# Optimization experiments

Measured on AMD Instinct MI355X. Metric: run time of the kernel, lower is better.

Reference implementation:

```python
import jax, jax.numpy as jnp
import numpy as np

BATCH, N_NEURONS = 4096, 4096
FEAT = 512
MAP_H, MAP_W = 256, 256
M = MAP_H * MAP_W
TAU_MEM = 20.0
THRESHOLD = 1.0
LR = 0.005          # stdp_params['learning_rate']
SIGMA = 2.0         # SOM neighborhood radius (grid units)
N_UPDATES = 3       # perceive() runs the SOM forward+update loop 3 times


def setup_inputs() -> dict:
    key = jax.random.key(0)
    k = jax.random.split(key, 6)
    return {
        "sensory_input": jax.random.uniform(k[0], (BATCH, N_NEURONS), dtype=jnp.float32),
        "W_in":  jax.random.normal(k[1], (N_NEURONS, FEAT), dtype=jnp.float32) * 0.02,
        "W_out": jax.random.normal(k[2], (FEAT, FEAT), dtype=jnp.float32) * 0.05,
        "proj_W": jax.random.normal(k[3], (FEAT, FEAT), dtype=jnp.float32) * 0.05,
        "proj_b": jax.random.normal(k[4], (FEAT,), dtype=jnp.float32) * 0.05,
        "som_w": jax.random.uniform(k[5], (M, FEAT), dtype=jnp.float32),
    }


def _grid_coords():
    yy, xx = jnp.meshgrid(jnp.arange(MAP_H, dtype=jnp.float32),
                          jnp.arange(MAP_W, dtype=jnp.float32), indexing="ij")
    return jnp.stack([yy.ravel(), xx.ravel()], axis=-1)  # [M, 2]


def reference(sensory_input, W_in, W_out, proj_W, proj_b, som_w):
    # --- CorticalColumn (single LIF step, prev state None -> v0 = 0) ---
    x = sensory_input.mean(axis=0)                  # [N] batch mean per perceive()
    current = x @ W_in                              # [FEAT] feedforward current
    v = current                                     # v = 0*decay + current
    spikes = (v >= THRESHOLD).astype(v.dtype)       # LIF threshold, hard reset
    v_after = jnp.where(spikes > 0, 0.0, v)
    out_ff = spikes @ W_out                         # column feedforward output [FEAT]

    # --- input projection + ReLU ---
    feat = jax.nn.relu(out_ff @ proj_W.T + proj_b)  # [FEAT]

    coords = _grid_coords()                         # [M, 2]

    def som_act(w):
        d2 = jnp.sum((w - feat) ** 2, axis=-1)      # [M] distance sweep (memory-bound)
        return jnp.exp(-d2 / (2.0 * FEAT))          # rate-coded activation

    def step(w, _):
        act = som_act(w)
        bmu = jnp.argmax(act)                       # best matching unit
        g2 = jnp.sum((coords - coords[bmu]) ** 2, axis=-1)
        nb = jnp.exp(-g2 / (2.0 * SIGMA ** 2))      # Gaussian neighborhood
        w = w + LR * nb[:, None] * (feat - w)       # STDP-style pull toward input
        return w, None

    som_w, _ = jax.lax.scan(step, som_w, None, length=N_UPDATES)

    final = som_act(som_w).reshape(MAP_H, MAP_W)    # final SOM activation map
    return final
```

## Files before the change

kernel.cpp:

```cpp
#include <hip/hip_runtime.h>

#define NN        4096
#define FEATN     512
#define LRC       0.005f


__global__ void k_colsum_part(const float* __restrict__ A, float* __restrict__ partial, int rpb) {
    int col = blockIdx.x * 1024 + threadIdx.x * 4;
    const float* p = A + (size_t)blockIdx.y * rpb * NN + col;
    float4 acc = make_float4(0.f, 0.f, 0.f, 0.f);
    for (int r = 0; r < rpb; r += 8) {
        #pragma unroll
        for (int u = 0; u < 8; ++u) {
            float4 v = *reinterpret_cast<const float4*>(p + (size_t)(r + u) * NN);
            acc.x += v.x; acc.y += v.y; acc.z += v.z; acc.w += v.w;
        }
    }
    *reinterpret_cast<float4*>(partial + (size_t)blockIdx.y * NN + col) = acc;
}

__global__ void k_colsum_fin(const float* __restrict__ partial, float* __restrict__ sumx,
                             float* __restrict__ current, float* __restrict__ outff,
                             unsigned long long* __restrict__ bmuKey, int chunks) {
    int col = blockIdx.x * 256 + threadIdx.x;
    float acc = 0.f;
    #pragma unroll 8
    for (int p = 0; p < chunks; ++p)
        acc += partial[(size_t)p * NN + col];
    sumx[col] = acc * (1.0f / 4096.0f);
    if (blockIdx.x == 0) { current[threadIdx.x] = 0.f; current[threadIdx.x + 256] = 0.f; }
    if (blockIdx.x == 1) { outff[threadIdx.x]   = 0.f; outff[threadIdx.x + 256]   = 0.f; }
    if (blockIdx.x == 2 && threadIdx.x == 0) *bmuKey = ~0ull;
}

__global__ void k_current(const float* __restrict__ Win, const float* __restrict__ sumx,
                          float* __restrict__ current) {
    int t  = blockIdx.y * 256 + threadIdx.x;
    int i0 = blockIdx.x * 64;
    float acc = 0.f;
    #pragma unroll 8
    for (int i = 0; i < 64; ++i)
        acc += sumx[i0 + i] * Win[(size_t)(i0 + i) * FEATN + t];
    atomicAdd(&current[t], acc);
}

__global__ void k_outff(const float* __restrict__ Wout, const float* __restrict__ current,
                        float* __restrict__ outff) {
    int t  = blockIdx.y * 256 + threadIdx.x;
    int k0 = blockIdx.x * 32;
    float acc = 0.f;
    for (int k = 0; k < 32; ++k) {
        if (current[k0 + k] >= 1.0f)
            acc += Wout[(size_t)(k0 + k) * FEATN + t];
    }
    atomicAdd(&outff[t], acc);
}

__global__ void k_feat(const float* __restrict__ projW, const float* __restrict__ projb,
                       const float* __restrict__ outff, float* __restrict__ feat) {
    int lane = threadIdx.x & 63;
    int j    = blockIdx.x * 4 + (threadIdx.x >> 6);
    const float4* row = reinterpret_cast<const float4*>(projW + (size_t)j * FEATN);
    const float4* v   = reinterpret_cast<const float4*>(outff);
    float4 a0 = row[lane],      b0 = v[lane];
    float4 a1 = row[lane + 64], b1 = v[lane + 64];
    float s = a0.x * b0.x + a0.y * b0.y + a0.z * b0.z + a0.w * b0.w
            + a1.x * b1.x + a1.y * b1.y + a1.z * b1.z + a1.w * b1.w;
    #pragma unroll
    for (int k = 32; k >= 1; k >>= 1) s += __shfl_xor(s, k, 64);
    if (lane == 0) {
        float f = s + projb[j];
        feat[j] = f > 0.f ? f : 0.f;
    }
}

__global__ void k_d2(const float* __restrict__ somw, const float* __restrict__ feat,
                     float* __restrict__ d2out, unsigned long long* __restrict__ bmuKey) {
    __shared__ float sf[FEATN];
    __shared__ unsigned long long smin[4];
    int tid = threadIdx.x;
    sf[tid]       = feat[tid];
    sf[tid + 256] = feat[tid + 256];
    __syncthreads();

    int wave = tid >> 6, lane = tid & 63;
    int base = blockIdx.x * 32 + wave * 8;
    const float4* fv = reinterpret_cast<const float4*>(sf);
    float4 f0 = fv[lane], f1 = fv[lane + 64];

    float4 va[8], vb[8];
    #pragma unroll
    for (int r = 0; r < 8; ++r) {
        const float4* row = reinterpret_cast<const float4*>(somw + (size_t)(base + r) * FEATN);
        va[r] = row[lane];
        vb[r] = row[lane + 64];
    }

    float s[8];
    #pragma unroll
    for (int r = 0; r < 8; ++r) {
        float d, acc = 0.f;
        d = va[r].x - f0.x; acc += d * d;
        d = va[r].y - f0.y; acc += d * d;
        d = va[r].z - f0.z; acc += d * d;
        d = va[r].w - f0.w; acc += d * d;
        d = vb[r].x - f1.x; acc += d * d;
        d = vb[r].y - f1.y; acc += d * d;
        d = vb[r].z - f1.z; acc += d * d;
        d = vb[r].w - f1.w; acc += d * d;
        s[r] = acc;
    }
    #pragma unroll
    for (int r = 0; r < 8; ++r) {
        #pragma unroll
        for (int k = 32; k >= 1; k >>= 1) s[r] += __shfl_xor(s[r], k, 64);
    }

    if (lane == 0) {
        float4 o0 = make_float4(s[0], s[1], s[2], s[3]);
        float4 o1 = make_float4(s[4], s[5], s[6], s[7]);
        *reinterpret_cast<float4*>(d2out + base)     = o0;
        *reinterpret_cast<float4*>(d2out + base + 4) = o1;
        unsigned long long kmin = ~0ull;
        #pragma unroll
        for (int r = 0; r < 8; ++r) {
            unsigned long long key =
                ((unsigned long long)__float_as_uint(s[r]) << 32) | (unsigned)(base + r);
            if (key < kmin) kmin = key;
        }
        smin[wave] = kmin;
    }
    __syncthreads();
    if (tid == 0) {
        unsigned long long k0 = smin[0];
        if (smin[1] < k0) k0 = smin[1];
        if (smin[2] < k0) k0 = smin[2];
        if (smin[3] < k0) k0 = smin[3];
        if (k0 < *(volatile unsigned long long*)bmuKey)
            atomicMin(bmuKey, k0);
    }
}

__global__ void k_final(float* __restrict__ out, const unsigned long long* __restrict__ bmuKey) {
    int m = blockIdx.x * 256 + threadIdx.x;
    unsigned long long key = *bmuKey;
    int bmu = (int)(key & 0xFFFFFFFFull);
    float dy = (float)(m >> 8)  - (float)(bmu >> 8);
    float dx = (float)(m & 255) - (float)(bmu & 255);
    float g2 = dy * dy + dx * dx;
    float nb = expf(-g2 * 0.125f);
    float fac = 1.0f - LRC * nb;
    float f2 = fac * fac;
    float f6 = f2 * f2 * f2;
    float d2 = out[m];
    out[m] = expf(-(d2 * f6) * (1.0f / 1024.0f));
}

extern "C" void kernel_launch(void* const* d_in, const int* in_sizes, int n_in,
                              void* d_out, int out_size, void* d_ws, size_t ws_size,
                              hipStream_t stream) {
    const float* sensory = (const float*)d_in[0];
    const float* Win     = (const float*)d_in[1];
    const float* Wout    = (const float*)d_in[2];
    const float* projW   = (const float*)d_in[3];
    const float* projb   = (const float*)d_in[4];
    const float* somw    = (const float*)d_in[5];
    float* out = (float*)d_out;

    char* ws = (char*)d_ws;
    float* sumx    = (float*)(ws);
    float* current = (float*)(ws + 16384);
    float* outff   = (float*)(ws + 18432);
    float* feat    = (float*)(ws + 20480);
    unsigned long long* bmuKey = (unsigned long long*)(ws + 22528);
    float* partial = (float*)(ws + 24576);

    int chunks = 128;
    while (chunks > 16 && ws_size < (size_t)24576 + (size_t)chunks * NN * 4) chunks >>= 1;
    int rpb = NN / chunks;

    hipLaunchKernelGGL(k_colsum_part, dim3(4, chunks), dim3(256), 0, stream, sensory, partial, rpb);
    hipLaunchKernelGGL(k_colsum_fin,  dim3(16),        dim3(256), 0, stream, partial, sumx, current, outff, bmuKey, chunks);
    hipLaunchKernelGGL(k_current,     dim3(64, 2),     dim3(256), 0, stream, Win, sumx, current);
    hipLaunchKernelGGL(k_outff,       dim3(16, 2),     dim3(256), 0, stream, Wout, current, outff);
    hipLaunchKernelGGL(k_feat,        dim3(128),       dim3(256), 0, stream, projW, projb, outff, feat);
    hipLaunchKernelGGL(k_d2,          dim3(2048),      dim3(256), 0, stream, somw, feat, out, bmuKey);
    hipLaunchKernelGGL(k_final,       dim3(256),       dim3(256), 0, stream, out, bmuKey);
}
```

Baseline: 277.3 us.

## Fuse front-end column kernels into one persistent kernel with grid barriers

Replaces the five front-end launches (column sum partials, final reduction, W_in matvec, W_out spike matvec, projection) with a single 256-block kernel that separates the phases with software grid barriers built on atomic counters and flags. The goal is to remove per-launch overhead and the inter-kernel gaps in the serial chain of small matvecs. Barrier counters are cleared each call with a memset. The partial-sum layout is fixed at 64 chunks, and the barriers only work if all 256 blocks are resident at once, which would deadlock otherwise.

```diff
diff --git a/kernel.cpp b/kernel.cpp
--- a/kernel.cpp
+++ b/kernel.cpp
@@ -1,76 +1,109 @@
 #include <hip/hip_runtime.h>
 
-#define NN        4096
-#define FEATN     512
-#define LRC       0.005f
-
-
-__global__ void k_colsum_part(const float* __restrict__ A, float* __restrict__ partial, int rpb) {
-    int col = blockIdx.x * 1024 + threadIdx.x * 4;
-    const float* p = A + (size_t)blockIdx.y * rpb * NN + col;
-    float4 acc = make_float4(0.f, 0.f, 0.f, 0.f);
-    for (int r = 0; r < rpb; r += 8) {
-        #pragma unroll
-        for (int u = 0; u < 8; ++u) {
-            float4 v = *reinterpret_cast<const float4*>(p + (size_t)(r + u) * NN);
-            acc.x += v.x; acc.y += v.y; acc.z += v.z; acc.w += v.w;
-        }
-    }
-    *reinterpret_cast<float4*>(partial + (size_t)blockIdx.y * NN + col) = acc;
-}
-
-__global__ void k_colsum_fin(const float* __restrict__ partial, float* __restrict__ sumx,
-                             float* __restrict__ current, float* __restrict__ outff,
-                             unsigned long long* __restrict__ bmuKey, int chunks) {
-    int col = blockIdx.x * 256 + threadIdx.x;
-    float acc = 0.f;
-    #pragma unroll 8
-    for (int p = 0; p < chunks; ++p)
-        acc += partial[(size_t)p * NN + col];
-    sumx[col] = acc * (1.0f / 4096.0f);
-    if (blockIdx.x == 0) { current[threadIdx.x] = 0.f; current[threadIdx.x + 256] = 0.f; }
-    if (blockIdx.x == 1) { outff[threadIdx.x]   = 0.f; outff[threadIdx.x + 256]   = 0.f; }
-    if (blockIdx.x == 2 && threadIdx.x == 0) *bmuKey = ~0ull;
-}
-
-__global__ void k_current(const float* __restrict__ Win, const float* __restrict__ sumx,
-                          float* __restrict__ current) {
-    int t  = blockIdx.y * 256 + threadIdx.x;
-    int i0 = blockIdx.x * 64;
-    float acc = 0.f;
-    #pragma unroll 8
-    for (int i = 0; i < 64; ++i)
-        acc += sumx[i0 + i] * Win[(size_t)(i0 + i) * FEATN + t];
-    atomicAdd(&current[t], acc);
-}
-
-__global__ void k_outff(const float* __restrict__ Wout, const float* __restrict__ current,
-                        float* __restrict__ outff) {
-    int t  = blockIdx.y * 256 + threadIdx.x;
-    int k0 = blockIdx.x * 32;
-    float acc = 0.f;
-    for (int k = 0; k < 32; ++k) {
-        if (current[k0 + k] >= 1.0f)
-            acc += Wout[(size_t)(k0 + k) * FEATN + t];
-    }
-    atomicAdd(&outff[t], acc);
-}
-
-__global__ void k_feat(const float* __restrict__ projW, const float* __restrict__ projb,
-                       const float* __restrict__ outff, float* __restrict__ feat) {
-    int lane = threadIdx.x & 63;
-    int j    = blockIdx.x * 4 + (threadIdx.x >> 6);
-    const float4* row = reinterpret_cast<const float4*>(projW + (size_t)j * FEATN);
-    const float4* v   = reinterpret_cast<const float4*>(outff);
-    float4 a0 = row[lane],      b0 = v[lane];
-    float4 a1 = row[lane + 64], b1 = v[lane + 64];
-    float s = a0.x * b0.x + a0.y * b0.y + a0.z * b0.z + a0.w * b0.w
-            + a1.x * b1.x + a1.y * b1.y + a1.z * b1.z + a1.w * b1.w;
-    #pragma unroll
-    for (int k = 32; k >= 1; k >>= 1) s += __shfl_xor(s, k, 64);
-    if (lane == 0) {
-        float f = s + projb[j];
-        feat[j] = f > 0.f ? f : 0.f;
+#define NNEUR 4096
+#define FEATN 512
+#define LRC   0.005f
+#define NBLK  256
+
+
+__device__ __forceinline__ void gbar(unsigned* bar, int k) {
+    __syncthreads();
+    if (threadIdx.x == 0) {
+        __threadfence();
+        unsigned prev = atomicAdd(&bar[k], 1u);
+        if (prev == NBLK - 1u) {
+            __hip_atomic_store(&bar[4 + k], 1u, __ATOMIC_RELEASE, __HIP_MEMORY_SCOPE_AGENT);
+        } else {
+            while (__hip_atomic_load(&bar[4 + k], __ATOMIC_ACQUIRE, __HIP_MEMORY_SCOPE_AGENT) == 0u)
+                __builtin_amdgcn_s_sleep(2);
+        }
+        __threadfence();
+    }
+    __syncthreads();
+}
+
+__global__ __launch_bounds__(256) void k_front(
+        const float* __restrict__ A,     const float* __restrict__ Win,
+        const float* __restrict__ Wout,  const float* __restrict__ projW,
+        const float* __restrict__ projb,
+        float* __restrict__ sumx, float* __restrict__ cur, float* __restrict__ outff,
+        float* __restrict__ feat, float* __restrict__ partial,
+        unsigned* __restrict__ bar, unsigned long long* __restrict__ bmuKey) {
+    const int b = blockIdx.x, tid = threadIdx.x;
+
+    {
+        int col = (b & 3) * 1024 + tid * 4;
+        const float* p = A + (size_t)(b >> 2) * 64 * NNEUR + col;
+        float4 acc = make_float4(0.f, 0.f, 0.f, 0.f);
+        for (int r = 0; r < 64; r += 8) {
+            #pragma unroll
+            for (int u = 0; u < 8; ++u) {
+                float4 v = *reinterpret_cast<const float4*>(p + (size_t)(r + u) * NNEUR);
+                acc.x += v.x; acc.y += v.y; acc.z += v.z; acc.w += v.w;
+            }
+        }
+        *reinterpret_cast<float4*>(partial + (size_t)(b >> 2) * NNEUR + col) = acc;
+    }
+    gbar(bar, 0);
+
+    if (b < 16) {
+        int col = b * 256 + tid;
+        float acc = 0.f;
+        #pragma unroll 8
+        for (int p = 0; p < 64; ++p)
+            acc += partial[(size_t)p * NNEUR + col];
+        sumx[col] = acc * (1.0f / 4096.0f);
+    } else if (b == 16) { cur[tid] = 0.f;   cur[tid + 256] = 0.f; }
+    else if (b == 17)   { outff[tid] = 0.f; outff[tid + 256] = 0.f; }
+    else if (b == 18 && tid == 0) *bmuKey = ~0ull;
+    gbar(bar, 1);
+
+    {
+        int r0 = b * 16;
+        float a0 = 0.f, a1 = 0.f;
+        #pragma unroll 4
+        for (int i = 0; i < 16; ++i) {
+            float s = sumx[r0 + i];
+            const float* row = Win + (size_t)(r0 + i) * FEATN;
+            a0 += s * row[tid];
+            a1 += s * row[tid + 256];
+        }
+        atomicAdd(&cur[tid], a0);
+        atomicAdd(&cur[tid + 256], a1);
+    }
+    gbar(bar, 2);
+
+    if (b < 128) {
+        int k0 = b * 4;
+        float a0 = 0.f, a1 = 0.f;
+        #pragma unroll
+        for (int i = 0; i < 4; ++i) {
+            if (cur[k0 + i] >= 1.0f) {
+                const float* row = Wout + (size_t)(k0 + i) * FEATN;
+                a0 += row[tid];
+                a1 += row[tid + 256];
+            }
+        }
+        atomicAdd(&outff[tid], a0);
+        atomicAdd(&outff[tid + 256], a1);
+    }
+    gbar(bar, 3);
+
+    if (b < 128) {
+        int lane = tid & 63;
+        int j = b * 4 + (tid >> 6);
+        const float4* row = reinterpret_cast<const float4*>(projW + (size_t)j * FEATN);
+        const float4* v   = reinterpret_cast<const float4*>(outff);
+        float4 a0 = row[lane],      b0 = v[lane];
+        float4 a1 = row[lane + 64], b1 = v[lane + 64];
+        float s = a0.x * b0.x + a0.y * b0.y + a0.z * b0.z + a0.w * b0.w
+                + a1.x * b1.x + a1.y * b1.y + a1.z * b1.z + a1.w * b1.w;
+        #pragma unroll
+        for (int k = 32; k >= 1; k >>= 1) s += __shfl_xor(s, k, 64);
+        if (lane == 0) {
+            float f = s + projb[j];
+            feat[j] = f > 0.f ? f : 0.f;
+        }
     }
 }
 
@@ -117,10 +150,8 @@
     }
 
     if (lane == 0) {
-        float4 o0 = make_float4(s[0], s[1], s[2], s[3]);
-        float4 o1 = make_float4(s[4], s[5], s[6], s[7]);
-        *reinterpret_cast<float4*>(d2out + base)     = o0;
-        *reinterpret_cast<float4*>(d2out + base + 4) = o1;
+        *reinterpret_cast<float4*>(d2out + base)     = make_float4(s[0], s[1], s[2], s[3]);
+        *reinterpret_cast<float4*>(d2out + base + 4) = make_float4(s[4], s[5], s[6], s[7]);
         unsigned long long kmin = ~0ull;
         #pragma unroll
         for (int r = 0; r < 8; ++r) {
@@ -159,6 +190,7 @@
 extern "C" void kernel_launch(void* const* d_in, const int* in_sizes, int n_in,
                               void* d_out, int out_size, void* d_ws, size_t ws_size,
                               hipStream_t stream) {
+    (void)in_sizes; (void)n_in; (void)out_size; (void)ws_size;
     const float* sensory = (const float*)d_in[0];
     const float* Win     = (const float*)d_in[1];
     const float* Wout    = (const float*)d_in[2];
@@ -169,21 +201,18 @@
 
     char* ws = (char*)d_ws;
     float* sumx    = (float*)(ws);
-    float* current = (float*)(ws + 16384);
+    float* cur     = (float*)(ws + 16384);
     float* outff   = (float*)(ws + 18432);
     float* feat    = (float*)(ws + 20480);
     unsigned long long* bmuKey = (unsigned long long*)(ws + 22528);
+    unsigned* bar  = (unsigned*)(ws + 22592);
     float* partial = (float*)(ws + 24576);
 
-    int chunks = 128;
-    while (chunks > 16 && ws_size < (size_t)24576 + (size_t)chunks * NN * 4) chunks >>= 1;
-    int rpb = NN / chunks;
-
-    hipLaunchKernelGGL(k_colsum_part, dim3(4, chunks), dim3(256), 0, stream, sensory, partial, rpb);
-    hipLaunchKernelGGL(k_colsum_fin,  dim3(16),        dim3(256), 0, stream, partial, sumx, current, outff, bmuKey, chunks);
-    hipLaunchKernelGGL(k_current,     dim3(64, 2),     dim3(256), 0, stream, Win, sumx, current);
-    hipLaunchKernelGGL(k_outff,       dim3(16, 2),     dim3(256), 0, stream, Wout, current, outff);
-    hipLaunchKernelGGL(k_feat,        dim3(128),       dim3(256), 0, stream, projW, projb, outff, feat);
-    hipLaunchKernelGGL(k_d2,          dim3(2048),      dim3(256), 0, stream, somw, feat, out, bmuKey);
-    hipLaunchKernelGGL(k_final,       dim3(256),       dim3(256), 0, stream, out, bmuKey);
-}
+    hipMemsetAsync(bar, 0, 32, stream);
+
+    hipLaunchKernelGGL(k_front, dim3(NBLK), dim3(256), 0, stream,
+                       sensory, Win, Wout, projW, projb,
+                       sumx, cur, outff, feat, partial, bar, bmuKey);
+    hipLaunchKernelGGL(k_d2,    dim3(2048), dim3(256), 0, stream, somw, feat, out, bmuKey);
+    hipLaunchKernelGGL(k_final, dim3(256),  dim3(256), 0, stream, out, bmuKey);
+}
```

Result: slower. 358.7 us (+29.4%).
